# Performance work log

Hardware: AMD Instinct MI355X
Metric: run time of the kernel (lower is better)

The kernel has to match this reference:

```python
import jax, jax.numpy as jnp
import numpy as np

N_NODES = 50000
N_EDGES = 800000
D_IN = 128
D_HID = 128
D_OUT = 128
BN_EPS = 1e-5


def _lin_params(key, d_out, d_in, bias=True):
    k1, k2 = jax.random.split(key)
    s = 1.0 / np.sqrt(d_in)
    W = jax.random.uniform(k1, (d_out, d_in), jnp.float32, -s, s)
    b = jax.random.uniform(k2, (d_out,), jnp.float32, -s, s) if bias else None
    return W, b


def setup_inputs() -> dict:
    key = jax.random.key(0)
    ks = jax.random.split(key, 10)
    x = jax.random.normal(ks[0], (N_NODES, D_IN), jnp.float32)
    edge_index = jax.random.randint(ks[1], (2, N_EDGES), 0, N_NODES, jnp.int32)
    Wl0, bl0 = _lin_params(ks[2], D_HID, D_IN)
    Wr0, _ = _lin_params(ks[3], D_HID, D_IN, bias=False)
    Wl1, bl1 = _lin_params(ks[4], D_HID, D_HID)
    Wr1, _ = _lin_params(ks[5], D_HID, D_HID, bias=False)
    Wl2, bl2 = _lin_params(ks[6], D_OUT, D_HID)
    Wr2, _ = _lin_params(ks[7], D_OUT, D_HID, bias=False)
    gamma1 = jnp.ones((D_HID,), jnp.float32)
    beta1 = jnp.zeros((D_HID,), jnp.float32)
    return dict(x=x, edge_index=edge_index,
                Wl0=Wl0, bl0=bl0, Wr0=Wr0,
                Wl1=Wl1, bl1=bl1, Wr1=Wr1,
                Wl2=Wl2, bl2=bl2, Wr2=Wr2,
                gamma1=gamma1, beta1=beta1)


def sage_conv(x, src, dst, Wl, bl, Wr):
    # gather messages from source nodes, mean-aggregate at destination nodes
    msg = x[src]                                                   # [E, d]
    agg = jax.ops.segment_sum(msg, dst, num_segments=N_NODES)      # [N, d]
    cnt = jax.ops.segment_sum(jnp.ones((src.shape[0],), x.dtype), dst,
                              num_segments=N_NODES)
    mean = agg / jnp.maximum(cnt, 1.0)[:, None]
    return mean @ Wl.T + bl + x @ Wr.T


def batch_norm(x, gamma, beta):
    mu = jnp.mean(x, axis=0)
    var = jnp.var(x, axis=0)
    return (x - mu) * jax.lax.rsqrt(var + BN_EPS) * gamma + beta


def reference(x, edge_index, Wl0, bl0, Wr0, Wl1, bl1, Wr1, Wl2, bl2, Wr2,
              gamma1, beta1):
    src, dst = edge_index[0], edge_index[1]
    h = jax.nn.relu(sage_conv(x, src, dst, Wl0, bl0, Wr0))
    h = sage_conv(h, src, dst, Wl1, bl1, Wr1)
    h = jax.nn.relu(batch_norm(h, gamma1, beta1))
    return sage_conv(h, src, dst, Wl2, bl2, Wr2)
```

## Files before the change

### kernel.cpp

```cpp
#include <hip/hip_runtime.h>
#include <hip/hip_bf16.h>
#include <cstdint>

#define N_NODES 50000
#define N_EDGES 800000
#define D 128
#define NBUCK 196
#define CAP 4608

typedef __attribute__((ext_vector_type(4))) float f32x4;
typedef __attribute__((ext_vector_type(8))) short s16x8;

__device__ __forceinline__ float bflo(uint32_t v) { return __uint_as_float(v << 16); }
__device__ __forceinline__ float bfhi(uint32_t v) { return __uint_as_float(v & 0xffff0000u); }
__device__ __forceinline__ uint32_t f2b(float f) {
    uint32_t x = __float_as_uint(f);
    uint32_t r = x + 0x7fffu + ((x >> 16) & 1u);
    return r >> 16;
}
__device__ __forceinline__ uint32_t pack2(float lo, float hi) {
    return f2b(lo) | (f2b(hi) << 16);
}

__global__ __launch_bounds__(256) void pb_k(const float* __restrict__ x,
                       const float* __restrict__ Wl0, const float* __restrict__ Wr0,
                       const float* __restrict__ Wl1, const float* __restrict__ Wr1,
                       const float* __restrict__ Wl2, const float* __restrict__ Wr2,
                       uint32_t* __restrict__ X0, uint32_t* __restrict__ Wc,
                       const int* __restrict__ src, const int* __restrict__ dst,
                       int* __restrict__ bcnt, uint2* __restrict__ ebuf)
{
    const int t = threadIdx.x;
    if (blockIdx.x < 512) {
        __shared__ int h[256], base[256], cur[256];
        h[t] = 0; cur[t] = 0;
        __syncthreads();
        const int chunk = (N_EDGES + 511) / 512;
        const int e0 = blockIdx.x * chunk;
        int e1 = e0 + chunk; if (e1 > N_EDGES) e1 = N_EDGES;
        for (int e = e0 + t; e < e1; e += 256) {
            int b = dst[e] >> 8;
            atomicAdd(&h[b], 1);
        }
        __syncthreads();
        if (t < NBUCK) base[t] = (h[t] > 0) ? atomicAdd(&bcnt[t], h[t]) : 0;
        __syncthreads();
        for (int e = e0 + t; e < e1; e += 256) {
            int s = src[e], d = dst[e];
            int b = d >> 8;
            int r = atomicAdd(&cur[b], 1);
            int pos = base[b] + r;
            if (pos < CAP) ebuf[b * CAP + pos] = make_uint2((uint32_t)s, (uint32_t)d);
        }
    } else {
        const int NX = N_NODES * D / 2;
        const int NW = 3 * 128 * 128;
        const int bid = blockIdx.x - 512;
        for (int i = bid * 256 + t; i < NX + NW; i += 2048 * 256) {
            if (i < NX) {
                const float2 v = reinterpret_cast<const float2*>(x)[i];
                X0[i] = pack2(v.x, v.y);
            } else {
                int j = i - NX;
                int l = j / 16384;
                int r = j % 16384;
                int n = r >> 7;
                int k2 = (r & 127) * 2;
                const float* Wl = (l == 0) ? Wl0 : (l == 1) ? Wl1 : Wl2;
                const float* Wr = (l == 0) ? Wr0 : (l == 1) ? Wr1 : Wr2;
                float a, b;
                if (k2 < 128) { a = Wl[n * 128 + k2];       b = Wl[n * 128 + k2 + 1]; }
                else          { a = Wr[n * 128 + k2 - 128]; b = Wr[n * 128 + k2 - 127]; }
                Wc[j] = pack2(a, b);
            }
        }
    }
}

__global__ __launch_bounds__(256) void csr_k(const uint2* __restrict__ ebuf,
                                             const int* __restrict__ bcnt,
                                             int* __restrict__ rowptr,
                                             int* __restrict__ adj)
{
    __shared__ int bs[256], cntL[256], offL[256], curL[256];
    const int b = blockIdx.x;
    const int t = threadIdx.x;
    const int n0 = b << 8;
    int bv = (t < NBUCK) ? bcnt[t] : 0;
    bs[t] = bv;
    __syncthreads();
    for (int d = 1; d < 256; d <<= 1) {
        int tmp = (t >= d) ? bs[t - d] : 0;
        __syncthreads();
        bs[t] += tmp;
        __syncthreads();
    }
    const int gbase = (b == 0) ? 0 : bs[b - 1];
    const int m = bcnt[b];
    cntL[t] = 0; curL[t] = 0;
    __syncthreads();
    const uint2* eb = ebuf + b * CAP;
    for (int i = t; i < m; i += 256)
        atomicAdd(&cntL[(int)eb[i].y - n0], 1);
    __syncthreads();
    int v = cntL[t];
    offL[t] = v;
    __syncthreads();
    for (int d = 1; d < 256; d <<= 1) {
        int tmp = (t >= d) ? offL[t - d] : 0;
        __syncthreads();
        offL[t] += tmp;
        __syncthreads();
    }
    int excl = offL[t] - v;
    int node = n0 + t;
    if (node < N_NODES) rowptr[node] = gbase + excl;
    if (b == NBUCK - 1 && t == 0) rowptr[N_NODES] = N_EDGES;
    __syncthreads();
    offL[t] = excl;
    __syncthreads();
    for (int i = t; i < m; i += 256) {
        uint2 e = eb[i];
        int d = (int)e.y - n0;
        int r = atomicAdd(&curL[d], 1);
        adj[gbase + offL[d] + r] = (int)e.x;
    }
}

template <int APPLYBN>
__global__ __launch_bounds__(256) void agg_k(const uint32_t* __restrict__ inB,
                                             const int* __restrict__ rowptr,
                                             const int* __restrict__ adj,
                                             uint32_t* __restrict__ meanb,
                                             const float* __restrict__ colsums,
                                             const float* __restrict__ gamma,
                                             const float* __restrict__ beta)
{
    const int wid = threadIdx.x >> 6;
    const int lane = threadIdx.x & 63;
    const int n = blockIdx.x * 4 + wid;
    const int sub = lane >> 4;
    const int col4 = lane & 15;

    float vsc[8], vsh[8];
    if constexpr (APPLYBN) {
        __shared__ float bnS[256];
        const int t = threadIdx.x;
        if (t < 128) {
            float mu  = colsums[t] * (1.0f / N_NODES);
            float var = colsums[128 + t] * (1.0f / N_NODES) - mu * mu;
            float sc  = gamma[t] * rsqrtf(var + 1e-5f);
            bnS[t] = sc;
            bnS[128 + t] = beta[t] - mu * sc;
        }
        __syncthreads();
#pragma unroll
        for (int k = 0; k < 8; ++k) {
            int c = col4 * 8 + k;
            vsc[k] = bnS[c]; vsh[k] = bnS[128 + c];
        }
    }
    if (n >= N_NODES) return;

    const int start = rowptr[n], end = rowptr[n + 1];
    float acc[8];
#pragma unroll
    for (int k = 0; k < 8; ++k) acc[k] = 0.f;

    for (int base = start; base < end; base += 64) {
        int cnt = end - base;
        if (cnt > 64) cnt = 64;
        int idx = (base + lane < end) ? adj[base + lane] : 0;
        for (int j = 0; j < cnt; j += 8) {
            int e0 = j + sub;
            int e1 = j + 4 + sub;
            int s0 = __shfl(idx, e0, 64);
            int s1 = __shfl(idx, e1, 64);
            bool v0 = e0 < cnt;
            bool v1 = e1 < cnt;
            uint4 a = *reinterpret_cast<const uint4*>(inB + (v0 ? s0 : 0) * 64 + col4 * 4);
            uint4 b = *reinterpret_cast<const uint4*>(inB + (v1 ? s1 : 0) * 64 + col4 * 4);
            if constexpr (APPLYBN) {
                float m0 = v0 ? 1.f : 0.f;
                float m1 = v1 ? 1.f : 0.f;
#define ACCBN(K, GA, GB) acc[K] += m0 * fmaxf(fmaf((GA), vsc[K], vsh[K]), 0.f) \
                                 + m1 * fmaxf(fmaf((GB), vsc[K], vsh[K]), 0.f)
                ACCBN(0, bflo(a.x), bflo(b.x)); ACCBN(1, bfhi(a.x), bfhi(b.x));
                ACCBN(2, bflo(a.y), bflo(b.y)); ACCBN(3, bfhi(a.y), bfhi(b.y));
                ACCBN(4, bflo(a.z), bflo(b.z)); ACCBN(5, bfhi(a.z), bfhi(b.z));
                ACCBN(6, bflo(a.w), bflo(b.w)); ACCBN(7, bfhi(a.w), bfhi(b.w));
#undef ACCBN
            } else {
                if (!v0) a = make_uint4(0, 0, 0, 0);
                if (!v1) b = make_uint4(0, 0, 0, 0);
                acc[0] += bflo(a.x); acc[1] += bfhi(a.x);
                acc[2] += bflo(a.y); acc[3] += bfhi(a.y);
                acc[4] += bflo(a.z); acc[5] += bfhi(a.z);
                acc[6] += bflo(a.w); acc[7] += bfhi(a.w);
                acc[0] += bflo(b.x); acc[1] += bfhi(b.x);
                acc[2] += bflo(b.y); acc[3] += bfhi(b.y);
                acc[4] += bflo(b.z); acc[5] += bfhi(b.z);
                acc[6] += bflo(b.w); acc[7] += bfhi(b.w);
            }
        }
    }

#pragma unroll
    for (int k = 0; k < 8; ++k) {
        acc[k] += __shfl_xor(acc[k], 16, 64);
        acc[k] += __shfl_xor(acc[k], 32, 64);
    }

    if (sub == 0) {
        int deg = end - start;
        float sc = 1.0f / (float)(deg > 0 ? deg : 1);
        uint4 w;
        w.x = pack2(acc[0] * sc, acc[1] * sc);
        w.y = pack2(acc[2] * sc, acc[3] * sc);
        w.z = pack2(acc[4] * sc, acc[5] * sc);
        w.w = pack2(acc[6] * sc, acc[7] * sc);
        *reinterpret_cast<uint4*>(meanb + n * 64 + col4 * 4) = w;
    }
}

__device__ __forceinline__ s16x8 bn8(uint4 u, const float* bnS, int cb) {
    uint32_t uu[4] = {u.x, u.y, u.z, u.w};
    uint32_t w[4];
#pragma unroll
    for (int i = 0; i < 4; ++i) {
        int c = cb + 2 * i;
        float lo = fmaxf(fmaf(bflo(uu[i]), bnS[c],     bnS[128 + c]),     0.f);
        float hi = fmaxf(fmaf(bfhi(uu[i]), bnS[c + 1], bnS[128 + c + 1]), 0.f);
        w[i] = pack2(lo, hi);
    }
    uint4 r = make_uint4(w[0], w[1], w[2], w[3]);
    return __builtin_bit_cast(s16x8, r);
}

template <int LAYER>
__global__ __launch_bounds__(256) void gemm_k(const uint32_t* __restrict__ meanb,
                                              const uint32_t* __restrict__ inB,
                                              const uint32_t* __restrict__ Wc,
                                              const float* __restrict__ bias,
                                              void* __restrict__ outp,
                                              float* __restrict__ colsums,
                                              const float* __restrict__ gamma,
                                              const float* __restrict__ beta)
{
    __shared__ uint32_t Bs[16384];
    __shared__ float extraS[256];
    const int t = threadIdx.x;
    const uint32_t* Wg = Wc + LAYER * 16384;
    {
        const int r = t >> 1;
        const int h = t & 1;
        const int sw = (r & 7) << 2;
#pragma unroll
        for (int q = 0; q < 16; ++q) {
            int off = h * 64 + q * 4;
            *reinterpret_cast<uint4*>(Bs + r * 128 + (off ^ sw)) =
                *reinterpret_cast<const uint4*>(Wg + r * 128 + off);
        }
    }
    if constexpr (LAYER == 1) {
        extraS[t] = 0.f;
    }
    if constexpr (LAYER == 2) {
        if (t < 128) {
            float mu  = colsums[t] * (1.0f / N_NODES);
            float var = colsums[128 + t] * (1.0f / N_NODES) - mu * mu;
            float sc  = gamma[t] * rsqrtf(var + 1e-5f);
            extraS[t] = sc;
            extraS[128 + t] = beta[t] - mu * sc;
        }
    }
    __syncthreads();

    const int lane = t & 63;
    const int wid = t >> 6;
    const int rowBase = blockIdx.x * 128 + wid * 32;
    const int l15 = lane & 15;
    const int kc = lane >> 4;
    int m0 = rowBase + l15;
    int m1 = m0 + 16;
    int m0c = m0 < N_NODES ? m0 : N_NODES - 1;
    int m1c = m1 < N_NODES ? m1 : N_NODES - 1;

    f32x4 acc[2][8];
#pragma unroll
    for (int a = 0; a < 2; ++a)
#pragma unroll
        for (int b = 0; b < 8; ++b) acc[a][b] = (f32x4){0.f, 0.f, 0.f, 0.f};

#pragma unroll
    for (int ks = 0; ks < 8; ++ks) {
        const int koff = (ks & 3) * 16 + kc * 4;
        s16x8 a0, a1;
        if (ks < 4) {
            a0 = *reinterpret_cast<const s16x8*>(meanb + m0c * 64 + koff);
            a1 = *reinterpret_cast<const s16x8*>(meanb + m1c * 64 + koff);
        } else {
            if constexpr (LAYER == 2) {
                const int cb = (ks & 3) * 32 + kc * 8;
                uint4 u0 = *reinterpret_cast<const uint4*>(inB + m0c * 64 + koff);
                uint4 u1 = *reinterpret_cast<const uint4*>(inB + m1c * 64 + koff);
                a0 = bn8(u0, extraS, cb);
                a1 = bn8(u1, extraS, cb);
            } else {
                a0 = *reinterpret_cast<const s16x8*>(inB + m0c * 64 + koff);
                a1 = *reinterpret_cast<const s16x8*>(inB + m1c * 64 + koff);
            }
        }
#pragma unroll
        for (int nf = 0; nf < 8; ++nf) {
            const int row = nf * 16 + l15;
            const int off = (ks * 16 + kc * 4) ^ ((row & 7) << 2);
            s16x8 b = *reinterpret_cast<const s16x8*>(Bs + row * 128 + off);
            acc[0][nf] = __builtin_amdgcn_mfma_f32_16x16x32_bf16(a0, b, acc[0][nf], 0, 0, 0);
            acc[1][nf] = __builtin_amdgcn_mfma_f32_16x16x32_bf16(a1, b, acc[1][nf], 0, 0, 0);
        }
    }

    const int rb = rowBase + (lane >> 4) * 4;
#pragma unroll
    for (int nf = 0; nf < 8; ++nf) {
        int col = nf * 16 + l15;
        float bia = bias[col];
        float s = 0.f, q = 0.f;
#pragma unroll
        for (int mf = 0; mf < 2; ++mf) {
#pragma unroll
            for (int r = 0; r < 4; ++r) {
                int row = rb + mf * 16 + r;
                if (row < N_NODES) {
                    float v = acc[mf][nf][r] + bia;
                    if (LAYER == 0) v = v > 0.f ? v : 0.f;
                    if (LAYER == 2)
                        ((float*)outp)[row * 128 + col] = v;
                    else
                        ((unsigned short*)outp)[row * 128 + col] = (unsigned short)f2b(v);
                    if constexpr (LAYER == 1) { s += v; q += v * v; }
                }
            }
        }
        if constexpr (LAYER == 1) {
            atomicAdd(&extraS[col], s);
            atomicAdd(&extraS[128 + col], q);
        }
    }
    if constexpr (LAYER == 1) {
        __syncthreads();
        if (t < 128) {
            atomicAdd(&colsums[t], extraS[t]);
            atomicAdd(&colsums[128 + t], extraS[128 + t]);
        }
    }
}

extern "C" void kernel_launch(void* const* d_in, const int* in_sizes, int n_in,
                              void* d_out, int out_size, void* d_ws, size_t ws_size,
                              hipStream_t stream)
{
    const float* x      = (const float*)d_in[0];
    const int*   ei     = (const int*)d_in[1];
    const float* Wl0    = (const float*)d_in[2];
    const float* bl0    = (const float*)d_in[3];
    const float* Wr0    = (const float*)d_in[4];
    const float* Wl1    = (const float*)d_in[5];
    const float* bl1    = (const float*)d_in[6];
    const float* Wr1    = (const float*)d_in[7];
    const float* Wl2    = (const float*)d_in[8];
    const float* bl2    = (const float*)d_in[9];
    const float* Wr2    = (const float*)d_in[10];
    const float* gamma1 = (const float*)d_in[11];
    const float* beta1  = (const float*)d_in[12];

    char* ws = (char*)d_ws;
    int*      bcnt    = (int*)(ws + 0);
    float*    colsums = (float*)(ws + 1024);
    int*      rowptr  = (int*)(ws + 4096);
    int*      adj     = (int*)(ws + 204160);
    uint2*    ebuf    = (uint2*)(ws + 3404160);
    uint32_t* bufA    = (uint32_t*)(ws + 10629504);
    uint32_t* bufB    = (uint32_t*)(ws + 23429504);
    uint32_t* bufC    = (uint32_t*)(ws + 36229504);
    uint32_t* Wc      = (uint32_t*)(ws + 49029504);
    uint32_t* X0 = bufA;
    uint32_t* MB = bufB;
    uint32_t* G1 = bufC;
    uint32_t* G2 = bufA;

    const int* srcI = ei;
    const int* dstI = ei + N_EDGES;

    hipMemsetAsync(ws, 0, 2048, stream);
    pb_k<<<2560, 256, 0, stream>>>(x, Wl0, Wr0, Wl1, Wr1, Wl2, Wr2, X0, Wc,
                                   srcI, dstI, bcnt, ebuf);
    csr_k<<<NBUCK, 256, 0, stream>>>(ebuf, bcnt, rowptr, adj);

    agg_k<0><<<12500, 256, 0, stream>>>(X0, rowptr, adj, MB, nullptr, nullptr, nullptr);
    gemm_k<0><<<391, 256, 0, stream>>>(MB, X0, Wc, bl0, (void*)G1, nullptr, nullptr, nullptr);
    agg_k<0><<<12500, 256, 0, stream>>>(G1, rowptr, adj, MB, nullptr, nullptr, nullptr);
    gemm_k<1><<<391, 256, 0, stream>>>(MB, G1, Wc, bl1, (void*)G2, colsums, nullptr, nullptr);
    agg_k<1><<<12500, 256, 0, stream>>>(G2, rowptr, adj, MB, colsums, gamma1, beta1);
    gemm_k<2><<<391, 256, 0, stream>>>(MB, G2, Wc, bl2, d_out, colsums, gamma1, beta1);
}
```

Measured before the change: 281.6 us.

## Fuse neighbor aggregation with MFMA GEMM per 64-node block via LDS

Merges the separate aggregation and GEMM kernels into one kernel per layer. Each block first mean-aggregates 64 nodes into a swizzled shared-memory tile, then runs bf16 MFMA against the weights, which are now read straight from global memory instead of being staged in LDS. This removes the global round trip of the mean buffer and three kernel launches. In exchange, each block holds only 16 rows per wave, weight reuse drops, and the serial per-node gather loop (16 nodes per wave) may lower parallelism and latency hiding.

```diff
diff --git a/kernel.cpp b/kernel.cpp
--- a/kernel.cpp
+++ b/kernel.cpp
@@ -127,102 +127,6 @@
     }
 }
 
-template <int APPLYBN>
-__global__ __launch_bounds__(256) void agg_k(const uint32_t* __restrict__ inB,
-                                             const int* __restrict__ rowptr,
-                                             const int* __restrict__ adj,
-                                             uint32_t* __restrict__ meanb,
-                                             const float* __restrict__ colsums,
-                                             const float* __restrict__ gamma,
-                                             const float* __restrict__ beta)
-{
-    const int wid = threadIdx.x >> 6;
-    const int lane = threadIdx.x & 63;
-    const int n = blockIdx.x * 4 + wid;
-    const int sub = lane >> 4;
-    const int col4 = lane & 15;
-
-    float vsc[8], vsh[8];
-    if constexpr (APPLYBN) {
-        __shared__ float bnS[256];
-        const int t = threadIdx.x;
-        if (t < 128) {
-            float mu  = colsums[t] * (1.0f / N_NODES);
-            float var = colsums[128 + t] * (1.0f / N_NODES) - mu * mu;
-            float sc  = gamma[t] * rsqrtf(var + 1e-5f);
-            bnS[t] = sc;
-            bnS[128 + t] = beta[t] - mu * sc;
-        }
-        __syncthreads();
-#pragma unroll
-        for (int k = 0; k < 8; ++k) {
-            int c = col4 * 8 + k;
-            vsc[k] = bnS[c]; vsh[k] = bnS[128 + c];
-        }
-    }
-    if (n >= N_NODES) return;
-
-    const int start = rowptr[n], end = rowptr[n + 1];
-    float acc[8];
-#pragma unroll
-    for (int k = 0; k < 8; ++k) acc[k] = 0.f;
-
-    for (int base = start; base < end; base += 64) {
-        int cnt = end - base;
-        if (cnt > 64) cnt = 64;
-        int idx = (base + lane < end) ? adj[base + lane] : 0;
-        for (int j = 0; j < cnt; j += 8) {
-            int e0 = j + sub;
-            int e1 = j + 4 + sub;
-            int s0 = __shfl(idx, e0, 64);
-            int s1 = __shfl(idx, e1, 64);
-            bool v0 = e0 < cnt;
-            bool v1 = e1 < cnt;
-            uint4 a = *reinterpret_cast<const uint4*>(inB + (v0 ? s0 : 0) * 64 + col4 * 4);
-            uint4 b = *reinterpret_cast<const uint4*>(inB + (v1 ? s1 : 0) * 64 + col4 * 4);
-            if constexpr (APPLYBN) {
-                float m0 = v0 ? 1.f : 0.f;
-                float m1 = v1 ? 1.f : 0.f;
-#define ACCBN(K, GA, GB) acc[K] += m0 * fmaxf(fmaf((GA), vsc[K], vsh[K]), 0.f) \
-                                 + m1 * fmaxf(fmaf((GB), vsc[K], vsh[K]), 0.f)
-                ACCBN(0, bflo(a.x), bflo(b.x)); ACCBN(1, bfhi(a.x), bfhi(b.x));
-                ACCBN(2, bflo(a.y), bflo(b.y)); ACCBN(3, bfhi(a.y), bfhi(b.y));
-                ACCBN(4, bflo(a.z), bflo(b.z)); ACCBN(5, bfhi(a.z), bfhi(b.z));
-                ACCBN(6, bflo(a.w), bflo(b.w)); ACCBN(7, bfhi(a.w), bfhi(b.w));
-#undef ACCBN
-            } else {
-                if (!v0) a = make_uint4(0, 0, 0, 0);
-                if (!v1) b = make_uint4(0, 0, 0, 0);
-                acc[0] += bflo(a.x); acc[1] += bfhi(a.x);
-                acc[2] += bflo(a.y); acc[3] += bfhi(a.y);
-                acc[4] += bflo(a.z); acc[5] += bfhi(a.z);
-                acc[6] += bflo(a.w); acc[7] += bfhi(a.w);
-                acc[0] += bflo(b.x); acc[1] += bfhi(b.x);
-                acc[2] += bflo(b.y); acc[3] += bfhi(b.y);
-                acc[4] += bflo(b.z); acc[5] += bfhi(b.z);
-                acc[6] += bflo(b.w); acc[7] += bfhi(b.w);
-            }
-        }
-    }
-
-#pragma unroll
-    for (int k = 0; k < 8; ++k) {
-        acc[k] += __shfl_xor(acc[k], 16, 64);
-        acc[k] += __shfl_xor(acc[k], 32, 64);
-    }
-
-    if (sub == 0) {
-        int deg = end - start;
-        float sc = 1.0f / (float)(deg > 0 ? deg : 1);
-        uint4 w;
-        w.x = pack2(acc[0] * sc, acc[1] * sc);
-        w.y = pack2(acc[2] * sc, acc[3] * sc);
-        w.z = pack2(acc[4] * sc, acc[5] * sc);
-        w.w = pack2(acc[6] * sc, acc[7] * sc);
-        *reinterpret_cast<uint4*>(meanb + n * 64 + col4 * 4) = w;
-    }
-}
-
 __device__ __forceinline__ s16x8 bn8(uint4 u, const float* bnS, int cb) {
     uint32_t uu[4] = {u.x, u.y, u.z, u.w};
     uint32_t w[4];
@@ -238,33 +142,24 @@
 }
 
 template <int LAYER>
-__global__ __launch_bounds__(256) void gemm_k(const uint32_t* __restrict__ meanb,
-                                              const uint32_t* __restrict__ inB,
-                                              const uint32_t* __restrict__ Wc,
-                                              const float* __restrict__ bias,
-                                              void* __restrict__ outp,
-                                              float* __restrict__ colsums,
-                                              const float* __restrict__ gamma,
-                                              const float* __restrict__ beta)
+__global__ __launch_bounds__(256) void fused_k(const uint32_t* __restrict__ inB,
+                                               const int* __restrict__ rowptr,
+                                               const int* __restrict__ adj,
+                                               const uint32_t* __restrict__ Wc,
+                                               const float* __restrict__ bias,
+                                               void* __restrict__ outp,
+                                               float* __restrict__ colsums,
+                                               const float* __restrict__ gamma,
+                                               const float* __restrict__ beta)
 {
-    __shared__ uint32_t Bs[16384];
+    __shared__ uint32_t meanS[4096];
     __shared__ float extraS[256];
     const int t = threadIdx.x;
-    const uint32_t* Wg = Wc + LAYER * 16384;
-    {
-        const int r = t >> 1;
-        const int h = t & 1;
-        const int sw = (r & 7) << 2;
-#pragma unroll
-        for (int q = 0; q < 16; ++q) {
-            int off = h * 64 + q * 4;
-            *reinterpret_cast<uint4*>(Bs + r * 128 + (off ^ sw)) =
-                *reinterpret_cast<const uint4*>(Wg + r * 128 + off);
-        }
-    }
-    if constexpr (LAYER == 1) {
-        extraS[t] = 0.f;
-    }
+    const int lane = t & 63;
+    const int wid = t >> 6;
+    const int blockBase = blockIdx.x * 64;
+
+    if constexpr (LAYER == 1) extraS[t] = 0.f;
     if constexpr (LAYER == 2) {
         if (t < 128) {
             float mu  = colsums[t] * (1.0f / N_NODES);
@@ -276,48 +171,111 @@
     }
     __syncthreads();
 
-    const int lane = t & 63;
-    const int wid = t >> 6;
-    const int rowBase = blockIdx.x * 128 + wid * 32;
+    const int sub = lane >> 4;
+    const int col4 = lane & 15;
+    float vsc[8], vsh[8];
+    if constexpr (LAYER == 2) {
+#pragma unroll
+        for (int k = 0; k < 8; ++k) {
+            int c = col4 * 8 + k;
+            vsc[k] = extraS[c]; vsh[k] = extraS[128 + c];
+        }
+    }
+    for (int i = 0; i < 16; ++i) {
+        const int rl = wid * 16 + i;
+        const int ni = blockBase + rl;
+        int start = 0, end = 0;
+        if (ni < N_NODES) { start = rowptr[ni]; end = rowptr[ni + 1]; }
+        float acc[8];
+#pragma unroll
+        for (int k = 0; k < 8; ++k) acc[k] = 0.f;
+        for (int base = start; base < end; base += 64) {
+            int cnt = end - base;
+            if (cnt > 64) cnt = 64;
+            int idx = (base + lane < end) ? adj[base + lane] : 0;
+            for (int j = 0; j < cnt; j += 8) {
+                int e0 = j + sub;
+                int e1 = j + 4 + sub;
+                int s0 = __shfl(idx, e0, 64);
+                int s1 = __shfl(idx, e1, 64);
+                bool v0 = e0 < cnt;
+                bool v1 = e1 < cnt;
+                uint4 a = *reinterpret_cast<const uint4*>(inB + (v0 ? s0 : 0) * 64 + col4 * 4);
+                uint4 b = *reinterpret_cast<const uint4*>(inB + (v1 ? s1 : 0) * 64 + col4 * 4);
+                if constexpr (LAYER == 2) {
+                    float m0 = v0 ? 1.f : 0.f;
+                    float m1 = v1 ? 1.f : 0.f;
+#define ACCBN(K, GA, GB) acc[K] += m0 * fmaxf(fmaf((GA), vsc[K], vsh[K]), 0.f) \
+                                 + m1 * fmaxf(fmaf((GB), vsc[K], vsh[K]), 0.f)
+                    ACCBN(0, bflo(a.x), bflo(b.x)); ACCBN(1, bfhi(a.x), bfhi(b.x));
+                    ACCBN(2, bflo(a.y), bflo(b.y)); ACCBN(3, bfhi(a.y), bfhi(b.y));
+                    ACCBN(4, bflo(a.z), bflo(b.z)); ACCBN(5, bfhi(a.z), bfhi(b.z));
+                    ACCBN(6, bflo(a.w), bflo(b.w)); ACCBN(7, bfhi(a.w), bfhi(b.w));
+#undef ACCBN
+                } else {
+                    if (!v0) a = make_uint4(0, 0, 0, 0);
+                    if (!v1) b = make_uint4(0, 0, 0, 0);
+                    acc[0] += bflo(a.x); acc[1] += bfhi(a.x);
+                    acc[2] += bflo(a.y); acc[3] += bfhi(a.y);
+                    acc[4] += bflo(a.z); acc[5] += bfhi(a.z);
+                    acc[6] += bflo(a.w); acc[7] += bfhi(a.w);
+                    acc[0] += bflo(b.x); acc[1] += bfhi(b.x);
+                    acc[2] += bflo(b.y); acc[3] += bfhi(b.y);
+                    acc[4] += bflo(b.z); acc[5] += bfhi(b.z);
+                    acc[6] += bflo(b.w); acc[7] += bfhi(b.w);
+                }
+            }
+        }
+#pragma unroll
+        for (int k = 0; k < 8; ++k) {
+            acc[k] += __shfl_xor(acc[k], 16, 64);
+            acc[k] += __shfl_xor(acc[k], 32, 64);
+        }
+        if (sub == 0) {
+            int deg = end - start;
+            float sc = 1.0f / (float)(deg > 0 ? deg : 1);
+            uint4 w;
+            w.x = pack2(acc[0] * sc, acc[1] * sc);
+            w.y = pack2(acc[2] * sc, acc[3] * sc);
+            w.z = pack2(acc[4] * sc, acc[5] * sc);
+            w.w = pack2(acc[6] * sc, acc[7] * sc);
+            const int off = (col4 * 4) ^ ((rl & 7) << 2);
+            *reinterpret_cast<uint4*>(meanS + rl * 64 + off) = w;
+        }
+    }
+    __syncthreads();
+
     const int l15 = lane & 15;
     const int kc = lane >> 4;
+    const int rowBase = blockBase + wid * 16;
+    const int rl0 = wid * 16 + l15;
     int m0 = rowBase + l15;
-    int m1 = m0 + 16;
     int m0c = m0 < N_NODES ? m0 : N_NODES - 1;
-    int m1c = m1 < N_NODES ? m1 : N_NODES - 1;
-
-    f32x4 acc[2][8];
-#pragma unroll
-    for (int a = 0; a < 2; ++a)
-#pragma unroll
-        for (int b = 0; b < 8; ++b) acc[a][b] = (f32x4){0.f, 0.f, 0.f, 0.f};
+    const uint32_t* Wg = Wc + LAYER * 16384;
+
+    f32x4 acc[8];
+#pragma unroll
+    for (int b = 0; b < 8; ++b) acc[b] = (f32x4){0.f, 0.f, 0.f, 0.f};
 
 #pragma unroll
     for (int ks = 0; ks < 8; ++ks) {
         const int koff = (ks & 3) * 16 + kc * 4;
-        s16x8 a0, a1;
+        s16x8 a0;
         if (ks < 4) {
-            a0 = *reinterpret_cast<const s16x8*>(meanb + m0c * 64 + koff);
-            a1 = *reinterpret_cast<const s16x8*>(meanb + m1c * 64 + koff);
+            a0 = *reinterpret_cast<const s16x8*>(meanS + rl0 * 64 + (koff ^ ((rl0 & 7) << 2)));
         } else {
             if constexpr (LAYER == 2) {
                 const int cb = (ks & 3) * 32 + kc * 8;
                 uint4 u0 = *reinterpret_cast<const uint4*>(inB + m0c * 64 + koff);
-                uint4 u1 = *reinterpret_cast<const uint4*>(inB + m1c * 64 + koff);
                 a0 = bn8(u0, extraS, cb);
-                a1 = bn8(u1, extraS, cb);
             } else {
                 a0 = *reinterpret_cast<const s16x8*>(inB + m0c * 64 + koff);
-                a1 = *reinterpret_cast<const s16x8*>(inB + m1c * 64 + koff);
             }
         }
 #pragma unroll
         for (int nf = 0; nf < 8; ++nf) {
-            const int row = nf * 16 + l15;
-            const int off = (ks * 16 + kc * 4) ^ ((row & 7) << 2);
-            s16x8 b = *reinterpret_cast<const s16x8*>(Bs + row * 128 + off);
-            acc[0][nf] = __builtin_amdgcn_mfma_f32_16x16x32_bf16(a0, b, acc[0][nf], 0, 0, 0);
-            acc[1][nf] = __builtin_amdgcn_mfma_f32_16x16x32_bf16(a1, b, acc[1][nf], 0, 0, 0);
+            s16x8 b = *reinterpret_cast<const s16x8*>(Wg + (nf * 16 + l15) * 128 + ks * 16 + kc * 4);
+            acc[nf] = __builtin_amdgcn_mfma_f32_16x16x32_bf16(a0, b, acc[nf], 0, 0, 0);
         }
     }
 
@@ -328,19 +286,16 @@
         float bia = bias[col];
         float s = 0.f, q = 0.f;
 #pragma unroll
-        for (int mf = 0; mf < 2; ++mf) {
-#pragma unroll
-            for (int r = 0; r < 4; ++r) {
-                int row = rb + mf * 16 + r;
-                if (row < N_NODES) {
-                    float v = acc[mf][nf][r] + bia;
-                    if (LAYER == 0) v = v > 0.f ? v : 0.f;
-                    if (LAYER == 2)
-                        ((float*)outp)[row * 128 + col] = v;
-                    else
-                        ((unsigned short*)outp)[row * 128 + col] = (unsigned short)f2b(v);
-                    if constexpr (LAYER == 1) { s += v; q += v * v; }
-                }
+        for (int r = 0; r < 4; ++r) {
+            int row = rb + r;
+            if (row < N_NODES) {
+                float v = acc[nf][r] + bia;
+                if (LAYER == 0) v = v > 0.f ? v : 0.f;
+                if (LAYER == 2)
+                    ((float*)outp)[row * 128 + col] = v;
+                else
+                    ((unsigned short*)outp)[row * 128 + col] = (unsigned short)f2b(v);
+                if constexpr (LAYER == 1) { s += v; q += v * v; }
             }
         }
         if constexpr (LAYER == 1) {
@@ -382,11 +337,9 @@
     int*      adj     = (int*)(ws + 204160);
     uint2*    ebuf    = (uint2*)(ws + 3404160);
     uint32_t* bufA    = (uint32_t*)(ws + 10629504);
-    uint32_t* bufB    = (uint32_t*)(ws + 23429504);
     uint32_t* bufC    = (uint32_t*)(ws + 36229504);
     uint32_t* Wc      = (uint32_t*)(ws + 49029504);
     uint32_t* X0 = bufA;
-    uint32_t* MB = bufB;
     uint32_t* G1 = bufC;
     uint32_t* G2 = bufA;
 
@@ -398,10 +351,11 @@
                                    srcI, dstI, bcnt, ebuf);
     csr_k<<<NBUCK, 256, 0, stream>>>(ebuf, bcnt, rowptr, adj);
 
-    agg_k<0><<<12500, 256, 0, stream>>>(X0, rowptr, adj, MB, nullptr, nullptr, nullptr);
-    gemm_k<0><<<391, 256, 0, stream>>>(MB, X0, Wc, bl0, (void*)G1, nullptr, nullptr, nullptr);
-    agg_k<0><<<12500, 256, 0, stream>>>(G1, rowptr, adj, MB, nullptr, nullptr, nullptr);
-    gemm_k<1><<<391, 256, 0, stream>>>(MB, G1, Wc, bl1, (void*)G2, colsums, nullptr, nullptr);
-    agg_k<1><<<12500, 256, 0, stream>>>(G2, rowptr, adj, MB, colsums, gamma1, beta1);
-    gemm_k<2><<<391, 256, 0, stream>>>(MB, G2, Wc, bl2, d_out, colsums, gamma1, beta1);
-}
+    const int NBLK = (N_NODES + 63) / 64;
+    fused_k<0><<<NBLK, 256, 0, stream>>>(X0, rowptr, adj, Wc, bl0, (void*)G1,
+                                         nullptr, nullptr, nullptr);
+    fused_k<1><<<NBLK, 256, 0, stream>>>(G1, rowptr, adj, Wc, bl1, (void*)G2,
+                                         colsums, nullptr, nullptr);
+    fused_k<2><<<NBLK, 256, 0, stream>>>(G2, rowptr, adj, Wc, bl2, d_out,
+                                         colsums, gamma1, beta1);
+}
```

After: 360.6 us. +28.1%, slower.
